# Optimization experiments

Measured on AMD Instinct MI355X. Metric: run time of the kernel, lower is better.

## Reference

```python
import jax, jax.numpy as jnp
import numpy as np
from functools import partial

WS = 11          # window size (safe for H=W=256)
SIGMA = 1.5
DATA_RANGE = 1.0
EPS = 1e-8


def _gaussian_window(ws: int, sigma: float, channels: int) -> jnp.ndarray:
    coords = jnp.arange(ws, dtype=jnp.float32) - ws // 2
    g = jnp.exp(-(coords ** 2) / (2.0 * sigma * sigma))
    g = g / (g.sum() + 1e-12)
    win2d = jnp.outer(g, g)                      # [ws, ws]
    # depthwise kernel: OIHW with O=C, I=1, feature_group_count=C
    return jnp.broadcast_to(win2d, (channels, 1, ws, ws))


def _depthwise_conv(x: jnp.ndarray, win: jnp.ndarray) -> jnp.ndarray:
    # x: [N, C, H, W]; same-padding depthwise Gaussian filter
    c = x.shape[1]
    pad = WS // 2
    return jax.lax.conv_general_dilated(
        x, win,
        window_strides=(1, 1),
        padding=[(pad, pad), (pad, pad)],
        dimension_numbers=('NCHW', 'OIHW', 'NCHW'),
        feature_group_count=c,
    )


def setup_inputs() -> dict:
    key = jax.random.key(0)
    k1, k2 = jax.random.split(key)
    shape = (8, 8, 3, 256, 256)  # [B, T, C, H, W]
    pred = jax.random.uniform(k1, shape, dtype=jnp.float32)
    target = jax.random.uniform(k2, shape, dtype=jnp.float32)
    return {"pred": pred, "target": target}


def reference(pred, target):
    pred = jnp.clip(pred.astype(jnp.float32), 0.0, 1.0)
    target = jnp.clip(target.astype(jnp.float32), 0.0, 1.0)
    B, T, C, H, W = pred.shape
    x = pred.reshape(B * T, C, H, W)
    y = target.reshape(B * T, C, H, W)

    win = _gaussian_window(WS, SIGMA, C)

    mu_x = _depthwise_conv(x, win)
    mu_y = _depthwise_conv(y, win)
    mu_x2 = mu_x * mu_x
    mu_y2 = mu_y * mu_y
    mu_xy = mu_x * mu_y

    sigma_x2 = jnp.maximum(_depthwise_conv(x * x, win) - mu_x2, 0.0)
    sigma_y2 = jnp.maximum(_depthwise_conv(y * y, win) - mu_y2, 0.0)
    sigma_xy = _depthwise_conv(x * y, win) - mu_xy

    C1 = (0.01 * DATA_RANGE) ** 2
    C2 = (0.03 * DATA_RANGE) ** 2
    num = (2.0 * mu_xy + C1) * (2.0 * sigma_xy + C2)
    den = (mu_x2 + mu_y2 + C1) * (sigma_x2 + sigma_y2 + C2)
    ssim_map = num / (den + EPS)
    ssim_map = jnp.nan_to_num(ssim_map, nan=0.0, posinf=0.0, neginf=0.0)
    return 1.0 - jnp.mean(ssim_map)
```

## Files before the change

kernel.cpp:

```cpp
#include <hip/hip_runtime.h>


typedef _Float16 h2 __attribute__((ext_vector_type(2)));
typedef __fp16 fp16v2 __attribute__((ext_vector_type(2)));

#define WSZ 11
#define RAD 5
#define IMH 256
#define IMW 256
#define BAND 4
#define NBANDS (IMH / BAND)
#define NPLANES 192
#define NWAVETOT (NPLANES * NBANDS)
#define WPB 4
#define NGRID (NWAVETOT / WPB)
#define NPIXF (192.0f * 256.0f * 256.0f)

#define GW0 0.001028381f
#define GW1 0.007598770f
#define GW2 0.036000770f
#define GW3 0.109360600f
#define GW4 0.213005700f
#define GW5 0.266011790f

__device__ __forceinline__ h2 pk_fma16(h2 a, h2 b, h2 c) {
    h2 d;
    asm("v_pk_fma_f16 %0, %1, %2, %3" : "=v"(d) : "v"(a), "v"(b), "v"(c));
    return d;
}
__device__ __forceinline__ h2 pk_mul16(h2 a, h2 b) {
    h2 d;
    asm("v_pk_mul_f16 %0, %1, %2" : "=v"(d) : "v"(a), "v"(b));
    return d;
}
__device__ __forceinline__ h2 pk_add16(h2 a, h2 b) {
    h2 d;
    asm("v_pk_add_f16 %0, %1, %2" : "=v"(d) : "v"(a), "v"(b));
    return d;
}

union H2U { h2 h; unsigned u; };
__device__ __forceinline__ unsigned h2u(h2 v) { H2U x; x.h = v; return x.u; }
__device__ __forceinline__ h2 u2h(unsigned v) { H2U x; x.u = v; return x.h; }

__device__ __forceinline__ h2 bperm(int idx, h2 v) {
    return u2h((unsigned)__builtin_amdgcn_ds_bpermute(idx, (int)h2u(v)));
}
__device__ __forceinline__ h2 albt(h2 hi, h2 lo) {
    return u2h(__builtin_amdgcn_alignbit(h2u(hi), h2u(lo), 16));
}

__device__ __forceinline__ h2 splat16(float s) {
    _Float16 t = (_Float16)s;
    return (h2){t, t};
}
__device__ __forceinline__ h2 zero16() { return (h2){(_Float16)0, (_Float16)0}; }

__device__ __forceinline__ h2 clip_pack(float a, float b) {
    a = fminf(fmaxf(a, 0.f), 1.f);
    b = fminf(fmaxf(b, 0.f), 1.f);
    fp16v2 r = __builtin_amdgcn_cvt_pkrtz(a, b);
    return __builtin_bit_cast(h2, r);
}

__global__ __launch_bounds__(256, 4) void ssim_band_kernel(
    const float* __restrict__ pred,
    const float* __restrict__ targ,
    float* __restrict__ partial)
{
    const int tid = threadIdx.x;
    const int lane = tid & 63;
    const int wid = tid >> 6;
    const int b = blockIdx.x * WPB + wid;
    const int plane = b >> 6;
    const int band = b & 63;
    const int r0 = band * BAND;

    const float4* __restrict__ pp =
        (const float4*)(pred + (size_t)plane * (IMH * IMW));
    const float4* __restrict__ tp =
        (const float4*)(targ + (size_t)plane * (IMH * IMW));

    const h2 W0 = splat16(GW0), W1 = splat16(GW1), W2 = splat16(GW2),
             W3 = splat16(GW3), W4 = splat16(GW4), W5 = splat16(GW5);
    const h2 wv16[WSZ] = {W0, W1, W2, W3, W4, W5, W4, W3, W2, W1, W0};

    const int iu1 = (lane - 1) << 2;
    const int iu2 = (lane - 2) << 2;
    const int id1 = (lane + 1) << 2;
    const int id2 = (lane + 2) << 2;
    const bool mu1 = lane >= 1;
    const bool mu2 = lane >= 2;
    const bool md1 = lane <= 62;
    const bool md2 = lane <= 61;

    h2 X[WSZ][2], Y[WSZ][2];

#pragma unroll
    for (int j = 0; j < 10; ++j) {
        const int r = r0 - RAD + j;
        float4 a = make_float4(0.f, 0.f, 0.f, 0.f);
        float4 c = a;
        if (r >= 0 && r < IMH) { a = pp[r * 64 + lane]; c = tp[r * 64 + lane]; }
        X[j][0] = clip_pack(a.x, a.y); X[j][1] = clip_pack(a.z, a.w);
        Y[j][0] = clip_pack(c.x, c.y); Y[j][1] = clip_pack(c.z, c.w);
    }

    float4 pa = make_float4(0.f, 0.f, 0.f, 0.f), pc = pa;
    {
        const int r = r0 + RAD;
        if (r < IMH) { pa = pp[r * 64 + lane]; pc = tp[r * 64 + lane]; }
    }

    const float C1 = 1e-4f, C2 = 9e-4f;
    float lsum = 0.f;

#pragma unroll 1
    for (int i = 0; i < BAND; ++i) {
        X[10][0] = clip_pack(pa.x, pa.y); X[10][1] = clip_pack(pa.z, pa.w);
        Y[10][0] = clip_pack(pc.x, pc.y); Y[10][1] = clip_pack(pc.z, pc.w);

        {
            const int rn = r0 + RAD + i + 1;
            if (rn < IMH) {
                pa = pp[rn * 64 + lane];
                pc = tp[rn * 64 + lane];
            } else {
                pa = make_float4(0.f, 0.f, 0.f, 0.f);
                pc = make_float4(0.f, 0.f, 0.f, 0.f);
            }
        }

        h2 vd[5][2];
#pragma unroll
        for (int p = 0; p < 2; ++p) {
            vd[0][p] = zero16(); vd[1][p] = zero16(); vd[2][p] = zero16();
            vd[3][p] = zero16(); vd[4][p] = zero16();
        }
#pragma unroll
        for (int k = 0; k < WSZ; ++k) {
            const h2 wk = wv16[k];
#pragma unroll
            for (int p = 0; p < 2; ++p) {
                const h2 x = X[k][p], y = Y[k][p];
                const h2 wx = pk_mul16(wk, x);
                const h2 wy = pk_mul16(wk, y);
                vd[0][p] = pk_add16(vd[0][p], wx);
                vd[1][p] = pk_add16(vd[1][p], wy);
                vd[2][p] = pk_fma16(wx, x, vd[2][p]);
                vd[3][p] = pk_fma16(wy, y, vd[3][p]);
                vd[4][p] = pk_fma16(wx, y, vd[4][p]);
            }
        }

        h2 hf[5][2];
#pragma unroll
        for (int ch = 0; ch < 5; ++ch) {
            const h2 H0 = vd[ch][0], H1 = vd[ch][1];
            h2 Gm3 = bperm(iu2, H1);
            h2 Gm2 = bperm(iu1, H0);
            h2 Gm1 = bperm(iu1, H1);
            h2 G2  = bperm(id1, H0);
            h2 G3  = bperm(id1, H1);
            h2 G4  = bperm(id2, H0);
            Gm3 = mu2 ? Gm3 : zero16();
            Gm2 = mu1 ? Gm2 : zero16();
            Gm1 = mu1 ? Gm1 : zero16();
            G2  = md1 ? G2  : zero16();
            G3  = md1 ? G3  : zero16();
            G4  = md2 ? G4  : zero16();
            const h2 P0  = albt(Gm2, Gm3);
            const h2 P1  = Gm2;
            const h2 P2  = albt(Gm1, Gm2);
            const h2 P3  = Gm1;
            const h2 P4  = albt(H0, Gm1);
            const h2 P5  = H0;
            const h2 P6  = albt(H1, H0);
            const h2 P7  = H1;
            const h2 P8  = albt(G2, H1);
            const h2 P9  = G2;
            const h2 P10 = albt(G3, G2);
            const h2 P11 = G3;
            const h2 P12 = albt(G4, G3);
            h2 a0 = pk_mul16(W0, P0);
            a0 = pk_fma16(W1, P1, a0);
            a0 = pk_fma16(W2, P2, a0);
            a0 = pk_fma16(W3, P3, a0);
            a0 = pk_fma16(W4, P4, a0);
            a0 = pk_fma16(W5, P5, a0);
            a0 = pk_fma16(W4, P6, a0);
            a0 = pk_fma16(W3, P7, a0);
            a0 = pk_fma16(W2, P8, a0);
            a0 = pk_fma16(W1, P9, a0);
            a0 = pk_fma16(W0, P10, a0);
            h2 a1 = pk_mul16(W0, P2);
            a1 = pk_fma16(W1, P3, a1);
            a1 = pk_fma16(W2, P4, a1);
            a1 = pk_fma16(W3, P5, a1);
            a1 = pk_fma16(W4, P6, a1);
            a1 = pk_fma16(W5, P7, a1);
            a1 = pk_fma16(W4, P8, a1);
            a1 = pk_fma16(W3, P9, a1);
            a1 = pk_fma16(W2, P10, a1);
            a1 = pk_fma16(W1, P11, a1);
            a1 = pk_fma16(W0, P12, a1);
            hf[ch][0] = a0;
            hf[ch][1] = a1;
        }

#pragma unroll
        for (int p = 0; p < 2; ++p) {
#pragma unroll
            for (int e = 0; e < 2; ++e) {
                const float mx = (float)hf[0][p][e];
                const float my = (float)hf[1][p][e];
                const float sxx = (float)hf[2][p][e];
                const float syy = (float)hf[3][p][e];
                const float sxy = (float)hf[4][p][e];
                const float mx2 = mx * mx, my2 = my * my, mxy = mx * my;
                const float vx = fmaxf(sxx - mx2, 0.f);
                const float vy = fmaxf(syy - my2, 0.f);
                const float vxy = sxy - mxy;
                const float num = fmaf(2.f, mxy, C1) * fmaf(2.f, vxy, C2);
                const float den = (mx2 + my2 + C1) * (vx + vy + C2) + 1e-8f;
                lsum += num * __builtin_amdgcn_rcpf(den);
            }
        }

#pragma unroll
        for (int k = 0; k < 10; ++k) {
            X[k][0] = X[k + 1][0]; X[k][1] = X[k + 1][1];
            Y[k][0] = Y[k + 1][0]; Y[k][1] = Y[k + 1][1];
        }
    }

#pragma unroll
    for (int off = 32; off > 0; off >>= 1)
        lsum += __shfl_xor(lsum, off, 64);

    __shared__ float wsum[WPB];
    if (lane == 0) wsum[wid] = lsum;
    __syncthreads();
    if (tid == 0)
        partial[blockIdx.x] = wsum[0] + wsum[1] + wsum[2] + wsum[3];
}

__global__ __launch_bounds__(256) void ssim_finalize(
    const float* __restrict__ partial,
    float* __restrict__ out)
{
    __shared__ float wsum[4];
    const int t = threadIdx.x;
    float s = 0.f;
    for (int i = t; i < NGRID; i += 256) s += partial[i];
#pragma unroll
    for (int off = 32; off > 0; off >>= 1)
        s += __shfl_xor(s, off, 64);
    const int lane = t & 63, wv = t >> 6;
    if (lane == 0) wsum[wv] = s;
    __syncthreads();
    if (t == 0)
        out[0] = 1.0f - (wsum[0] + wsum[1] + wsum[2] + wsum[3]) / NPIXF;
}

extern "C" void kernel_launch(void* const* d_in, const int* in_sizes, int n_in,
                              void* d_out, int out_size, void* d_ws, size_t ws_size,
                              hipStream_t stream) {
    const float* pred = (const float*)d_in[0];
    const float* targ = (const float*)d_in[1];
    float* out = (float*)d_out;
    float* part = (float*)d_ws;

    ssim_band_kernel<<<NGRID, 256, 0, stream>>>(pred, targ, part);
    ssim_finalize<<<1, 256, 0, stream>>>(part, out);
}
```

Measured before the change: 156.6 us.

## Filter sum/difference channels to cut Gaussian convolutions from five to four

Rewrites the SSIM statistics in terms of s=x+y and d=x-y, so only four blurred channels (mean and second moment of s and d) are needed instead of five, which removes one vertical and one horizontal filter pass including its cross-lane permutes. The row window becomes a ring buffer indexed modulo the window size, and the band loop is fully unrolled so the indices are compile-time and the per-row register shift disappears. The final SSIM expression is rebuilt from the four channels. It drops the per-channel clamp on each variance, and forming s and d in fp16 with a difference of squares may lose precision.

```diff
diff --git a/kernel.cpp b/kernel.cpp
--- a/kernel.cpp
+++ b/kernel.cpp
@@ -84,6 +84,7 @@
     const h2 W0 = splat16(GW0), W1 = splat16(GW1), W2 = splat16(GW2),
              W3 = splat16(GW3), W4 = splat16(GW4), W5 = splat16(GW5);
     const h2 wv16[WSZ] = {W0, W1, W2, W3, W4, W5, W4, W3, W2, W1, W0};
+    const h2 M2 = splat16(-2.0f);
 
     const int iu1 = (lane - 1) << 2;
     const int iu2 = (lane - 2) << 2;
@@ -94,7 +95,7 @@
     const bool md1 = lane <= 62;
     const bool md2 = lane <= 61;
 
-    h2 X[WSZ][2], Y[WSZ][2];
+    h2 RS[WSZ][2], RD[WSZ][2];
 
 #pragma unroll
     for (int j = 0; j < 10; ++j) {
@@ -102,8 +103,12 @@
         float4 a = make_float4(0.f, 0.f, 0.f, 0.f);
         float4 c = a;
         if (r >= 0 && r < IMH) { a = pp[r * 64 + lane]; c = tp[r * 64 + lane]; }
-        X[j][0] = clip_pack(a.x, a.y); X[j][1] = clip_pack(a.z, a.w);
-        Y[j][0] = clip_pack(c.x, c.y); Y[j][1] = clip_pack(c.z, c.w);
+        const h2 x0 = clip_pack(a.x, a.y), x1 = clip_pack(a.z, a.w);
+        const h2 y0 = clip_pack(c.x, c.y), y1 = clip_pack(c.z, c.w);
+        RS[j][0] = pk_add16(x0, y0);
+        RS[j][1] = pk_add16(x1, y1);
+        RD[j][0] = pk_fma16(M2, y0, RS[j][0]);
+        RD[j][1] = pk_fma16(M2, y1, RS[j][1]);
     }
 
     float4 pa = make_float4(0.f, 0.f, 0.f, 0.f), pc = pa;
@@ -115,10 +120,17 @@
     const float C1 = 1e-4f, C2 = 9e-4f;
     float lsum = 0.f;
 
-#pragma unroll 1
+#pragma unroll
     for (int i = 0; i < BAND; ++i) {
-        X[10][0] = clip_pack(pa.x, pa.y); X[10][1] = clip_pack(pa.z, pa.w);
-        Y[10][0] = clip_pack(pc.x, pc.y); Y[10][1] = clip_pack(pc.z, pc.w);
+        const int sIn = (i + 10) % WSZ;
+        {
+            const h2 x0 = clip_pack(pa.x, pa.y), x1 = clip_pack(pa.z, pa.w);
+            const h2 y0 = clip_pack(pc.x, pc.y), y1 = clip_pack(pc.z, pc.w);
+            RS[sIn][0] = pk_add16(x0, y0);
+            RS[sIn][1] = pk_add16(x1, y1);
+            RD[sIn][0] = pk_fma16(M2, y0, RS[sIn][0]);
+            RD[sIn][1] = pk_fma16(M2, y1, RS[sIn][1]);
+        }
 
         {
             const int rn = r0 + RAD + i + 1;
@@ -131,31 +143,31 @@
             }
         }
 
-        h2 vd[5][2];
+        h2 vd[4][2];
 #pragma unroll
         for (int p = 0; p < 2; ++p) {
-            vd[0][p] = zero16(); vd[1][p] = zero16(); vd[2][p] = zero16();
-            vd[3][p] = zero16(); vd[4][p] = zero16();
+            vd[0][p] = zero16(); vd[1][p] = zero16();
+            vd[2][p] = zero16(); vd[3][p] = zero16();
         }
 #pragma unroll
         for (int k = 0; k < WSZ; ++k) {
+            const int sl = (i + k) % WSZ;
             const h2 wk = wv16[k];
 #pragma unroll
             for (int p = 0; p < 2; ++p) {
-                const h2 x = X[k][p], y = Y[k][p];
-                const h2 wx = pk_mul16(wk, x);
-                const h2 wy = pk_mul16(wk, y);
-                vd[0][p] = pk_add16(vd[0][p], wx);
-                vd[1][p] = pk_add16(vd[1][p], wy);
-                vd[2][p] = pk_fma16(wx, x, vd[2][p]);
-                vd[3][p] = pk_fma16(wy, y, vd[3][p]);
-                vd[4][p] = pk_fma16(wx, y, vd[4][p]);
+                const h2 s = RS[sl][p], d = RD[sl][p];
+                const h2 ws = pk_mul16(wk, s);
+                const h2 wd = pk_mul16(wk, d);
+                vd[0][p] = pk_add16(vd[0][p], ws);
+                vd[1][p] = pk_add16(vd[1][p], wd);
+                vd[2][p] = pk_fma16(ws, s, vd[2][p]);
+                vd[3][p] = pk_fma16(wd, d, vd[3][p]);
             }
         }
 
-        h2 hf[5][2];
-#pragma unroll
-        for (int ch = 0; ch < 5; ++ch) {
+        h2 hf[4][2];
+#pragma unroll
+        for (int ch = 0; ch < 4; ++ch) {
             const h2 H0 = vd[ch][0], H1 = vd[ch][1];
             h2 Gm3 = bperm(iu2, H1);
             h2 Gm2 = bperm(iu1, H0);
@@ -212,25 +224,20 @@
         for (int p = 0; p < 2; ++p) {
 #pragma unroll
             for (int e = 0; e < 2; ++e) {
-                const float mx = (float)hf[0][p][e];
-                const float my = (float)hf[1][p][e];
-                const float sxx = (float)hf[2][p][e];
-                const float syy = (float)hf[3][p][e];
-                const float sxy = (float)hf[4][p][e];
-                const float mx2 = mx * mx, my2 = my * my, mxy = mx * my;
-                const float vx = fmaxf(sxx - mx2, 0.f);
-                const float vy = fmaxf(syy - my2, 0.f);
-                const float vxy = sxy - mxy;
-                const float num = fmaf(2.f, mxy, C1) * fmaf(2.f, vxy, C2);
-                const float den = (mx2 + my2 + C1) * (vx + vy + C2) + 1e-8f;
+                const float ms = (float)hf[0][p][e];
+                const float md = (float)hf[1][p][e];
+                const float Ss = (float)hf[2][p][e];
+                const float Sd = (float)hf[3][p][e];
+                const float P = ms * ms, Q = md * md;
+                const float mxy2 = 0.5f * (P - Q);
+                const float m2s  = 0.5f * (P + Q);
+                const float Ssum = 0.5f * (Ss + Sd);
+                const float ssum = fmaxf(Ssum - m2s, 0.f);
+                const float sxy2 = fmaf(0.5f, Ss - Sd, -mxy2);
+                const float num = (mxy2 + C1) * (sxy2 + C2);
+                const float den = fmaf(m2s + C1, ssum + C2, 1e-8f);
                 lsum += num * __builtin_amdgcn_rcpf(den);
             }
-        }
-
-#pragma unroll
-        for (int k = 0; k < 10; ++k) {
-            X[k][0] = X[k + 1][0]; X[k][1] = X[k + 1][1];
-            Y[k][0] = Y[k + 1][0]; Y[k][1] = Y[k + 1][1];
         }
     }
 
```

Result: faster. 149.9 us (-4.3%).
